# Optimization experiments

Measured on AMD Instinct MI355X. Metric: run time of the kernel, lower is better.

## Reference

```python
import jax, jax.numpy as jnp
import numpy as np

B, S, H = 1, 2048, 2048
NH, KVH = 32, 8
HD = H // NH
GROUPS = NH // KVH
ROPE_THETA = 10000.0


def _rope(x):
    # x: (b, s, heads, head_dim); HF-style rotate-half RoPE
    d = x.shape[-1]
    s = x.shape[1]
    inv_freq = 1.0 / (ROPE_THETA ** (jnp.arange(0, d, 2, dtype=jnp.float32) / d))
    t = jnp.arange(s, dtype=jnp.float32)
    freqs = jnp.einsum('s,f->sf', t, inv_freq)          # (s, d/2)
    emb = jnp.concatenate([freqs, freqs], axis=-1)       # (s, d)
    cos = jnp.cos(emb)[None, :, None, :].astype(x.dtype)
    sin = jnp.sin(emb)[None, :, None, :].astype(x.dtype)
    x1, x2 = x[..., : d // 2], x[..., d // 2:]
    rot = jnp.concatenate([-x2, x1], axis=-1)
    return x * cos + rot * sin


def setup_inputs() -> dict:
    key = jax.random.key(0)
    ks = jax.random.split(key, 6)
    scale = 0.02
    hidden_states = jax.random.normal(ks[0], (B, S, H), dtype=jnp.float32)
    Wq = jax.random.normal(ks[1], (H, NH, HD), dtype=jnp.float32) * scale
    Wk = jax.random.normal(ks[2], (H, KVH, HD), dtype=jnp.float32) * scale
    Wv = jax.random.normal(ks[3], (H, KVH, HD), dtype=jnp.float32) * scale
    Wo = jax.random.normal(ks[4], (H, H), dtype=jnp.float32) * scale
    # causal additive mask (b,1,s,s): 0 on/below diagonal, large negative above
    causal = jnp.tril(jnp.ones((S, S), dtype=bool))
    attention_mask = jnp.where(causal, 0.0, -1e9).astype(jnp.float32)[None, None]
    return {"hidden_states": hidden_states, "Wq": Wq, "Wk": Wk, "Wv": Wv,
            "Wo": Wo, "attention_mask": attention_mask}


def reference(hidden_states, Wq, Wk, Wv, Wo, attention_mask):
    b, s, _ = hidden_states.shape
    q = jnp.einsum('bsh,hnd->bsnd', hidden_states, Wq)   # (b,s,NH,HD)
    k = jnp.einsum('bsh,hnd->bsnd', hidden_states, Wk)   # (b,s,KVH,HD)
    v = jnp.einsum('bsh,hnd->bsnd', hidden_states, Wv)   # (b,s,KVH,HD)
    q = _rope(q)
    k = _rope(k)
    # GQA: tile kv heads along head axis (tf.tile semantics)
    k = jnp.tile(k, (1, 1, GROUPS, 1))                   # (b,s,NH,HD)
    v = jnp.tile(v, (1, 1, GROUPS, 1))
    # scores: 'aecd,abcd->acbe' -> (b, heads, q_len, k_len)
    scores = jnp.einsum('bend,bqnd->bnqe', k, q) / jnp.sqrt(
        jnp.asarray(HD, dtype=q.dtype))
    scores = scores + attention_mask
    scores = jnp.maximum(scores, jnp.finfo(scores.dtype).min)
    probs = jax.nn.softmax(scores, axis=-1)
    attn = jnp.einsum('bnqe,bend->bqnd', probs, v)       # (b,s,NH,HD)
    attn = attn.reshape(b, s, H)
    return jnp.einsum('bsh,hd->bsd', attn, Wo)
```

## Files before the change

kernel.cpp:

```cpp
#include <hip/hip_runtime.h>
#include <stdint.h>

typedef unsigned short u16;
typedef uint32_t u32;
typedef uint64_t u64;
typedef float f32x4 __attribute__((ext_vector_type(4)));
typedef float f32x16 __attribute__((ext_vector_type(16)));
typedef __bf16 bf16x8 __attribute__((ext_vector_type(8)));

#define S_LEN 2048
#define HID 2048
#define N_HEADS 32
#define KV_HEADS 8
#define HEAD_DIM 64
#define QKV_COLS 3072
#define QSCALE 0.18033688011112042f

__device__ __forceinline__ u16 f2b(float x) {
  union { float f; uint32_t u; } c; c.f = x;
  uint32_t u = (c.u + 0x7fffu + ((c.u >> 16) & 1u)) >> 16;
  return (u16)u;
}
__device__ __forceinline__ float b2f(u16 v) {
  union { uint32_t u; float f; } c; c.u = ((uint32_t)v) << 16;
  return c.f;
}
__device__ __forceinline__ u32 pkbf(float e, float o) {
  union { float f; u32 u; } a, b; a.f = e; b.f = o;
  return __builtin_amdgcn_perm(b.u, a.u, 0x07060302u);
}

#define GLL16(gptr, lptr)                                                      \
  __builtin_amdgcn_global_load_lds(                                            \
      (__attribute__((address_space(1))) void*)(gptr),                         \
      (__attribute__((address_space(3))) void*)(lptr), 16, 0, 0)

__global__ __launch_bounds__(256) void prep_fused(const float* __restrict__ Wq,
                                                  const float* __restrict__ Wk,
                                                  const float* __restrict__ Wv,
                                                  const float* __restrict__ Wo,
                                                  const float* __restrict__ hs,
                                                  u16* __restrict__ WqkvT,
                                                  u16* __restrict__ WoT,
                                                  u16* __restrict__ X) {
  const int b = blockIdx.x;
  const int t = threadIdx.x;
  if (b < 10240) {
    __shared__ float tile[32][33];
    const float* in;
    u16* out;
    int C, bx, by;
    if (b < 4096) { in = Wq; out = WqkvT; C = 2048; bx = b & 63; by = b >> 6; }
    else if (b < 5120) { int bb = b - 4096; in = Wk; out = WqkvT + 2048 * 2048; C = 512; bx = bb & 15; by = bb >> 4; }
    else if (b < 6144) { int bb = b - 5120; in = Wv; out = WqkvT + 2048 * 2048 + 512 * 2048; C = 512; bx = bb & 15; by = bb >> 4; }
    else { int bb = b - 6144; in = Wo; out = WoT; C = 2048; bx = bb & 63; by = bb >> 6; }
    const int tx = t & 31, ty = t >> 5;
    const int c0 = bx * 32, r0 = by * 32;
#pragma unroll
    for (int i = 0; i < 32; i += 8)
      tile[ty + i][tx] = in[(size_t)(r0 + ty + i) * C + c0 + tx];
    __syncthreads();
#pragma unroll
    for (int i = 0; i < 32; i += 8)
      out[(size_t)(c0 + ty + i) * 2048 + r0 + tx] = f2b(tile[tx][ty + i]);
  } else {
    int i = (b - 10240) * 256 + t;
    float4 v = reinterpret_cast<const float4*>(hs)[i];
    ushort4 o;
    o.x = f2b(v.x); o.y = f2b(v.y); o.z = f2b(v.z); o.w = f2b(v.w);
    reinterpret_cast<ushort4*>(X)[i] = o;
  }
}

__global__ void transpose_bf16(const u16* __restrict__ in, int istride,
                               u16* __restrict__ out, int R, int C) {
  __shared__ u16 tile[32][33];
  int c0 = blockIdx.x * 32, r0 = blockIdx.y * 32;
  int tx = threadIdx.x, ty = threadIdx.y;
#pragma unroll
  for (int i = 0; i < 32; i += 8)
    tile[ty + i][tx] = in[(size_t)(r0 + ty + i) * istride + c0 + tx];
  __syncthreads();
#pragma unroll
  for (int i = 0; i < 32; i += 8)
    out[(size_t)(c0 + ty + i) * R + r0 + tx] = tile[tx][ty + i];
}

__global__ __launch_bounds__(256) void gemm128s(const u16* __restrict__ A,
                                                const u16* __restrict__ BT,
                                                float* __restrict__ Cp,
                                                int M, int N, int K, int ksplit) {
  __shared__ __align__(16) u16 As[128 * 64];
  __shared__ __align__(16) u16 Bs[128 * 64];
  const int t = threadIdx.x;
  const int w = t >> 6, l = t & 63;
  const int lr = l & 15, lk = l >> 4;
  const int wr = w >> 1, wc = w & 1;
  const int m0 = blockIdx.x * 128, n0 = blockIdx.y * 128;
  const int z = blockIdx.z;
  const int kspan = K / ksplit;
  const int kBeg = z * kspan, kEnd = kBeg + kspan;
  Cp += (size_t)z * M * N;

  f32x4 acc[4][4];
#pragma unroll
  for (int m = 0; m < 4; ++m)
#pragma unroll
    for (int n = 0; n < 4; ++n)
      acc[m][n] = (f32x4){0.f, 0.f, 0.f, 0.f};

  const u16* aSrc = A + (size_t)(m0 + t / 8) * K + (t % 8) * 8;
  const u16* bSrc = BT + (size_t)(n0 + t / 8) * K + (t % 8) * 8;
  char* aDst = (char*)As + w * 1024;
  char* bDst = (char*)Bs + w * 1024;

  for (int k0 = kBeg; k0 < kEnd; k0 += 64) {
#pragma unroll
    for (int i = 0; i < 4; ++i)
      GLL16(aSrc + (size_t)i * 32 * K + k0, aDst + i * 4096);
#pragma unroll
    for (int i = 0; i < 4; ++i)
      GLL16(bSrc + (size_t)i * 32 * K + k0, bDst + i * 4096);
    __syncthreads();
#pragma unroll
    for (int kk = 0; kk < 2; ++kk) {
      bf16x8 af[4], bfr[4];
#pragma unroll
      for (int m = 0; m < 4; ++m)
        af[m] = *(const bf16x8*)&As[(wr * 64 + m * 16 + lr) * 64 + kk * 32 + lk * 8];
#pragma unroll
      for (int n = 0; n < 4; ++n)
        bfr[n] = *(const bf16x8*)&Bs[(wc * 64 + n * 16 + lr) * 64 + kk * 32 + lk * 8];
#pragma unroll
      for (int m = 0; m < 4; ++m)
#pragma unroll
        for (int n = 0; n < 4; ++n)
          acc[m][n] = __builtin_amdgcn_mfma_f32_16x16x32_bf16(af[m], bfr[n], acc[m][n], 0, 0, 0);
    }
    __syncthreads();
  }
#pragma unroll
  for (int m = 0; m < 4; ++m)
#pragma unroll
    for (int n = 0; n < 4; ++n) {
      int row0 = m0 + wr * 64 + m * 16 + lk * 4;
      int col = n0 + wc * 64 + n * 16 + lr;
#pragma unroll
      for (int r = 0; r < 4; ++r)
        Cp[(size_t)(row0 + r) * N + col] = acc[m][n][r];
    }
}

__global__ __launch_bounds__(256) void post_qkv(const float* __restrict__ P0,
                                                const float* __restrict__ P1,
                                                u16* __restrict__ QKV) {
  int idx = blockIdx.x * 256 + threadIdx.x;
  int s = idx / 1536, j = idx - s * 1536;
  const float* r0 = P0 + (size_t)s * QKV_COLS;
  const float* r1 = P1 + (size_t)s * QKV_COLS;
  u16* o = QKV + (size_t)s * QKV_COLS;
  if (j < 1280) {
    int hbase, i;
    float scale;
    if (j < 1024) { hbase = (j >> 5) * 64; i = j & 31; scale = QSCALE; }
    else { int jj = j - 1024; hbase = 2048 + (jj >> 5) * 64; i = jj & 31; scale = 1.0f; }
    int c1 = hbase + i, c2 = c1 + 32;
    float inv = __expf(-(float)i * (9.210340371976184f / 32.0f));
    float f = (float)s * inv;
    float sn, cs;
    sincosf(f, &sn, &cs);
    float x1 = r0[c1] + r1[c1], x2 = r0[c2] + r1[c2];
    o[c1] = f2b((x1 * cs - x2 * sn) * scale);
    o[c2] = f2b((x2 * cs + x1 * sn) * scale);
  } else {
    int c = 2560 + (j - 1280) * 2;
    *(u32*)(o + c) = pkbf(r0[c] + r1[c], r0[c + 1] + r1[c + 1]);
  }
}

__global__ __launch_bounds__(256) void post_out(const float* __restrict__ P0,
                                                const float* __restrict__ P1,
                                                float* __restrict__ out) {
  int i = blockIdx.x * 256 + threadIdx.x;
  float4 a = reinterpret_cast<const float4*>(P0)[i];
  float4 b = reinterpret_cast<const float4*>(P1)[i];
  a.x += b.x; a.y += b.y; a.z += b.z; a.w += b.w;
  reinterpret_cast<float4*>(out)[i] = a;
}

__global__ __launch_bounds__(256) void attn_kernel(const u16* __restrict__ QKV,
                                                   const u16* __restrict__ Vt,
                                                   u16* __restrict__ At) {
  __shared__ __align__(16) u16 scratch[4][32 * 64];
  const int t = threadIdx.x;
  const int w = t >> 6, l = t & 63;
  const int lq = l & 31;
  const int hi = l >> 5;
  const int b = blockIdx.x;
  const int qt = (b < 256) ? (63 - (b >> 3)) : ((b - 256) >> 3);
  const int head = (b & 7) * 4 + w;
  const int kvh = head & (KV_HEADS - 1);
  const int qbase = qt * 32;
  char* pb = (char*)scratch[w];
  const int swrow = lq * 128;
  const int swx = (lq & 7) << 4;

  bf16x8 qf[4];
  {
    const u16* qp = QKV + (size_t)(qbase + lq) * QKV_COLS + head * HEAD_DIM + hi * 8;
#pragma unroll
    for (int jj = 0; jj < 4; ++jj) qf[jj] = *(const bf16x8*)(qp + jj * 16);
  }
  const u16* Kb = QKV + HID + kvh * HEAD_DIM;
  const u16* Vb = Vt + (size_t)(kvh * HEAD_DIM) * S_LEN;

  f32x16 oacc0, oacc1;
#pragma unroll
  for (int i = 0; i < 16; ++i) { oacc0[i] = 0.f; oacc1[i] = 0.f; }
  float m_run = -1e30f;
  float l_run = 0.f;

  auto loadK = [&](int kv0, bf16x8* k0, bf16x8* k1) {
    const u16* kp = Kb + (size_t)(kv0 + lq) * QKV_COLS + hi * 8;
#pragma unroll
    for (int jj = 0; jj < 4; ++jj) {
      k0[jj] = *(const bf16x8*)(kp + jj * 16);
      k1[jj] = *(const bf16x8*)(kp + (size_t)32 * QKV_COLS + jj * 16);
    }
  };

  auto tile = [&](int kv0, const bf16x8* kf0, const bf16x8* kf1, bool mask0, bool mask1) {
    f32x16 s0, s1;
#pragma unroll
    for (int i = 0; i < 16; ++i) { s0[i] = 0.f; s1[i] = 0.f; }
#pragma unroll
    for (int jj = 0; jj < 4; ++jj)
      s0 = __builtin_amdgcn_mfma_f32_32x32x16_bf16(kf0[jj], qf[jj], s0, 0, 0, 0);
#pragma unroll
    for (int jj = 0; jj < 4; ++jj)
      s1 = __builtin_amdgcn_mfma_f32_32x32x16_bf16(kf1[jj], qf[jj], s1, 0, 0, 0);
    bf16x8 vf0[4], vf1[4];
    const u16* vp = Vb + (size_t)lq * S_LEN + kv0 + hi * 8;
#pragma unroll
    for (int ks = 0; ks < 4; ++ks) {
      vf0[ks] = *(const bf16x8*)(vp + ks * 16);
      vf1[ks] = *(const bf16x8*)(vp + (size_t)32 * S_LEN + ks * 16);
    }
    if (mask0) {
      const int c = kv0 - qbase;
#pragma unroll
      for (int r = 0; r < 16; ++r) {
        int kvr = (r & 3) + 8 * (r >> 2) + 4 * hi + c;
        s0[r] = (kvr > lq) ? -1e30f : s0[r];
      }
    }
    if (mask1) {
      const int c = kv0 + 32 - qbase;
#pragma unroll
      for (int r = 0; r < 16; ++r) {
        int kvr = (r & 3) + 8 * (r >> 2) + 4 * hi + c;
        s1[r] = (kvr > lq) ? -1e30f : s1[r];
      }
    }
    float mx[16];
#pragma unroll
    for (int r = 0; r < 16; ++r) mx[r] = fmaxf(s0[r], s1[r]);
#pragma unroll
    for (int st = 8; st >= 1; st >>= 1)
#pragma unroll
      for (int r = 0; r < st; ++r) mx[r] = fmaxf(mx[r], mx[r + st]);
    float pm = mx[0];
    pm = fmaxf(pm, __shfl_xor(pm, 32));
    if (!__all(pm <= m_run + 8.f)) {
      float mnew = fmaxf(m_run, pm);
      float esc = exp2f(m_run - mnew);
      m_run = mnew;
      l_run *= esc;
#pragma unroll
      for (int i = 0; i < 16; ++i) { oacc0[i] *= esc; oacc1[i] *= esc; }
    }
#pragma unroll
    for (int r = 0; r < 16; ++r) {
      s0[r] = exp2f(s0[r] - m_run);
      s1[r] = exp2f(s1[r] - m_run);
    }
    float ls[16];
#pragma unroll
    for (int r = 0; r < 16; ++r) ls[r] = s0[r] + s1[r];
#pragma unroll
    for (int st = 8; st >= 1; st >>= 1)
#pragma unroll
      for (int r = 0; r < st; ++r) ls[r] += ls[r + st];
    l_run += ls[0];
#pragma unroll
    for (int sb = 0; sb < 2; ++sb)
#pragma unroll
      for (int g = 0; g < 4; ++g) {
        u32 w0 = sb ? pkbf(s1[4 * g + 0], s1[4 * g + 1]) : pkbf(s0[4 * g + 0], s0[4 * g + 1]);
        u32 w1 = sb ? pkbf(s1[4 * g + 2], s1[4 * g + 3]) : pkbf(s0[4 * g + 2], s0[4 * g + 3]);
        int kvb2 = (32 * sb + 8 * g + 4 * hi) * 2;
        *(u64*)(pb + swrow + (kvb2 ^ swx)) = (u64)w0 | ((u64)w1 << 32);
      }
    asm volatile("s_waitcnt lgkmcnt(0)" ::: "memory");
    __builtin_amdgcn_sched_barrier(0);
    bf16x8 pa[4];
#pragma unroll
    for (int ks = 0; ks < 4; ++ks)
      pa[ks] = *(const bf16x8*)(pb + swrow + ((32 * ks + 16 * hi) ^ swx));
    asm volatile("" ::: "memory");
#pragma unroll
    for (int ks = 0; ks < 4; ++ks) {
      oacc0 = __builtin_amdgcn_mfma_f32_32x32x16_bf16(vf0[ks], pa[ks], oacc0, 0, 0, 0);
      oacc1 = __builtin_amdgcn_mfma_f32_32x32x16_bf16(vf1[ks], pa[ks], oacc1, 0, 0, 0);
    }
  };

  const int NTF = qt >> 1;
  bf16x8 ka0[4], ka1[4], kb0[4], kb1[4];
  loadK(0, ka0, ka1);
  int tl = 0;
  for (; tl + 2 <= NTF; tl += 2) {
    loadK((tl + 1) * 64, kb0, kb1);
    tile(tl * 64, ka0, ka1, false, false);
    loadK((tl + 2) * 64, ka0, ka1);
    tile((tl + 1) * 64, kb0, kb1, false, false);
  }
  if (tl < NTF) {
    loadK((tl + 1) * 64, kb0, kb1);
    tile(tl * 64, ka0, ka1, false, false);
    tile(NTF * 64, kb0, kb1, (qt & 1) == 0, true);
  } else {
    tile(NTF * 64, ka0, ka1, (qt & 1) == 0, true);
  }

  float l_tot = l_run + __shfl_xor(l_run, 32);
  float inv = 1.0f / l_tot;
  asm volatile("" ::: "memory");
#pragma unroll
  for (int dt = 0; dt < 2; ++dt) {
#pragma unroll
    for (int j = 0; j < 8; ++j) {
      int d = dt * 32 + 2 * (j & 1) + 8 * (j >> 1) + 4 * hi;
      float e = (dt ? oacc1[2 * j] : oacc0[2 * j]) * inv;
      float o = (dt ? oacc1[2 * j + 1] : oacc0[2 * j + 1]) * inv;
      *(u32*)(pb + swrow + ((d * 2) ^ swx)) = pkbf(e, o);
    }
  }
  asm volatile("s_waitcnt lgkmcnt(0)" ::: "memory");
  __builtin_amdgcn_sched_barrier(0);
#pragma unroll
  for (int pass = 0; pass < 4; ++pass) {
    int qq = pass * 8 + (l >> 3);
    int coff = (l & 7) * 16;
    f32x4 v = *(const f32x4*)(pb + qq * 128 + (coff ^ ((qq & 7) << 4)));
    *(f32x4*)&At[(size_t)(qbase + qq) * HID + head * HEAD_DIM + (l & 7) * 8] = v;
  }
}

extern "C" void kernel_launch(void* const* d_in, const int* in_sizes, int n_in,
                              void* d_out, int out_size, void* d_ws, size_t ws_size,
                              hipStream_t stream) {
  const float* hs = (const float*)d_in[0];
  const float* Wq = (const float*)d_in[1];
  const float* Wk = (const float*)d_in[2];
  const float* Wv = (const float*)d_in[3];
  const float* Wo = (const float*)d_in[4];

  char* ws = (char*)d_ws;
  const size_t MB = 1024 * 1024;
  u16* X      = (u16*)(ws + 0 * MB);
  u16* WqkvT  = (u16*)(ws + 8 * MB);
  u16* WoT    = (u16*)(ws + 20 * MB);
  u16* QKV    = (u16*)(ws + 28 * MB);
  u16* Vt     = (u16*)(ws + 40 * MB);
  u16* At     = (u16*)(ws + 42 * MB);
  float* QKVp = (float*)(ws + 50 * MB);
  float* Op   = (float*)(ws + 50 * MB);

  prep_fused<<<14336, 256, 0, stream>>>(Wq, Wk, Wv, Wo, hs, WqkvT, WoT, X);
  gemm128s<<<dim3(16, 24, 2), 256, 0, stream>>>(X, WqkvT, QKVp, 2048, QKV_COLS, 2048, 2);
  post_qkv<<<12288, 256, 0, stream>>>(QKVp, QKVp + (size_t)2048 * QKV_COLS, QKV);
  transpose_bf16<<<dim3(16, 64), dim3(32, 8), 0, stream>>>(QKV + HID + 512, QKV_COLS, Vt, 2048, 512);
  attn_kernel<<<dim3(512), 256, 0, stream>>>(QKV, Vt, At);
  gemm128s<<<dim3(16, 16, 2), 256, 0, stream>>>(At, WoT, Op, 2048, 2048, 2048, 2);
  post_out<<<4096, 256, 0, stream>>>(Op, Op + (size_t)2048 * 2048, (float*)d_out);
}
```

Before: 293.0 us.

## Split KV loop across four waves per head with LDS softmax merge

Before, each block ran four heads, one per wave, and each wave walked the full causal KV range for its 32-query tile. Now each block handles one (query tile, head) pair, and its four waves take interleaved 64-key tiles. Partial max, sum and output accumulators are merged through LDS by wave 0 (a split-K flash-decoding style reduction). The grid grows from 512 to 2048 blocks, which shortens the critical path of long causal rows and balances load better. The cost is extra LDS traffic, a block barrier, a serial merge on one wave, and loss of the explicit K register double-buffering.

```diff
diff --git a/kernel.cpp b/kernel.cpp
--- a/kernel.cpp
+++ b/kernel.cpp
@@ -191,17 +191,18 @@
 __global__ __launch_bounds__(256) void attn_kernel(const u16* __restrict__ QKV,
                                                    const u16* __restrict__ Vt,
                                                    u16* __restrict__ At) {
-  __shared__ __align__(16) u16 scratch[4][32 * 64];
+  __shared__ __align__(16) char slot[4][8192];
+  __shared__ float ml[4][2][64];
   const int t = threadIdx.x;
   const int w = t >> 6, l = t & 63;
   const int lq = l & 31;
   const int hi = l >> 5;
   const int b = blockIdx.x;
-  const int qt = (b < 256) ? (63 - (b >> 3)) : ((b - 256) >> 3);
-  const int head = (b & 7) * 4 + w;
+  const int qt = 63 - (b >> 5);
+  const int head = b & 31;
   const int kvh = head & (KV_HEADS - 1);
   const int qbase = qt * 32;
-  char* pb = (char*)scratch[w];
+  char* pb = (char*)slot[w];
   const int swrow = lq * 128;
   const int swx = (lq & 7) << 4;
 
@@ -220,16 +221,19 @@
   float m_run = -1e30f;
   float l_run = 0.f;
 
-  auto loadK = [&](int kv0, bf16x8* k0, bf16x8* k1) {
+  const int NT = (qt >> 1) + 1;
+  for (int j = w; j < NT; j += 4) {
+    const int kv0 = j * 64;
+    const bool tail = (j == NT - 1);
+    const bool mask0 = tail && ((qt & 1) == 0);
+    const bool mask1 = tail;
     const u16* kp = Kb + (size_t)(kv0 + lq) * QKV_COLS + hi * 8;
+    bf16x8 kf0[4], kf1[4];
 #pragma unroll
     for (int jj = 0; jj < 4; ++jj) {
-      k0[jj] = *(const bf16x8*)(kp + jj * 16);
-      k1[jj] = *(const bf16x8*)(kp + (size_t)32 * QKV_COLS + jj * 16);
-    }
-  };
-
-  auto tile = [&](int kv0, const bf16x8* kf0, const bf16x8* kf1, bool mask0, bool mask1) {
+      kf0[jj] = *(const bf16x8*)(kp + jj * 16);
+      kf1[jj] = *(const bf16x8*)(kp + (size_t)32 * QKV_COLS + jj * 16);
+    }
     f32x16 s0, s1;
 #pragma unroll
     for (int i = 0; i < 16; ++i) { s0[i] = 0.f; s1[i] = 0.f; }
@@ -313,36 +317,54 @@
       oacc0 = __builtin_amdgcn_mfma_f32_32x32x16_bf16(vf0[ks], pa[ks], oacc0, 0, 0, 0);
       oacc1 = __builtin_amdgcn_mfma_f32_32x32x16_bf16(vf1[ks], pa[ks], oacc1, 0, 0, 0);
     }
-  };
-
-  const int NTF = qt >> 1;
-  bf16x8 ka0[4], ka1[4], kb0[4], kb1[4];
-  loadK(0, ka0, ka1);
-  int tl = 0;
-  for (; tl + 2 <= NTF; tl += 2) {
-    loadK((tl + 1) * 64, kb0, kb1);
-    tile(tl * 64, ka0, ka1, false, false);
-    loadK((tl + 2) * 64, ka0, ka1);
-    tile((tl + 1) * 64, kb0, kb1, false, false);
-  }
-  if (tl < NTF) {
-    loadK((tl + 1) * 64, kb0, kb1);
-    tile(tl * 64, ka0, ka1, false, false);
-    tile(NTF * 64, kb0, kb1, (qt & 1) == 0, true);
-  } else {
-    tile(NTF * 64, ka0, ka1, (qt & 1) == 0, true);
-  }
-
-  float l_tot = l_run + __shfl_xor(l_run, 32);
-  float inv = 1.0f / l_tot;
-  asm volatile("" ::: "memory");
+  }
+
+  ml[w][0][l] = m_run;
+  ml[w][1][l] = l_run;
+  {
+    f32x4* os = (f32x4*)slot[w];
+#pragma unroll
+    for (int i = 0; i < 4; ++i) {
+      os[i * 64 + l] = (f32x4){oacc0[4 * i], oacc0[4 * i + 1], oacc0[4 * i + 2], oacc0[4 * i + 3]};
+      os[(4 + i) * 64 + l] = (f32x4){oacc1[4 * i], oacc1[4 * i + 1], oacc1[4 * i + 2], oacc1[4 * i + 3]};
+    }
+  }
+  __syncthreads();
+  if (w != 0) return;
+
+  float mw[4], sc[4];
+#pragma unroll
+  for (int w2 = 0; w2 < 4; ++w2) mw[w2] = ml[w2][0][l];
+  float m = fmaxf(fmaxf(mw[0], mw[1]), fmaxf(mw[2], mw[3]));
+  float ltot = 0.f;
+#pragma unroll
+  for (int w2 = 0; w2 < 4; ++w2) {
+    sc[w2] = exp2f(mw[w2] - m);
+    float lw = ml[w2][1][l];
+    float lx = ml[w2][1][l ^ 32];
+    ltot += (lw + lx) * sc[w2];
+  }
+  float inv = 1.0f / ltot;
+  f32x4 O[8];
+#pragma unroll
+  for (int i = 0; i < 8; ++i) O[i] = (f32x4){0.f, 0.f, 0.f, 0.f};
+#pragma unroll
+  for (int w2 = 0; w2 < 4; ++w2) {
+    const f32x4* os = (const f32x4*)slot[w2];
+#pragma unroll
+    for (int i = 0; i < 8; ++i) {
+      f32x4 v = os[i * 64 + l];
+      O[i][0] += v[0] * sc[w2]; O[i][1] += v[1] * sc[w2];
+      O[i][2] += v[2] * sc[w2]; O[i][3] += v[3] * sc[w2];
+    }
+  }
 #pragma unroll
   for (int dt = 0; dt < 2; ++dt) {
 #pragma unroll
     for (int j = 0; j < 8; ++j) {
       int d = dt * 32 + 2 * (j & 1) + 8 * (j >> 1) + 4 * hi;
-      float e = (dt ? oacc1[2 * j] : oacc0[2 * j]) * inv;
-      float o = (dt ? oacc1[2 * j + 1] : oacc0[2 * j + 1]) * inv;
+      float e = O[dt * 4 + (j >> 1)][2 * (j & 1)] * inv;
+      float o = O[dt * 4 + (j >> 1)][2 * (j & 1) + 1] * inv;
       *(u32*)(pb + swrow + ((d * 2) ^ swx)) = pkbf(e, o);
     }
   }
@@ -381,7 +403,7 @@
   gemm128s<<<dim3(16, 24, 2), 256, 0, stream>>>(X, WqkvT, QKVp, 2048, QKV_COLS, 2048, 2);
   post_qkv<<<12288, 256, 0, stream>>>(QKVp, QKVp + (size_t)2048 * QKV_COLS, QKV);
   transpose_bf16<<<dim3(16, 64), dim3(32, 8), 0, stream>>>(QKV + HID + 512, QKV_COLS, Vt, 2048, 512);
-  attn_kernel<<<dim3(512), 256, 0, stream>>>(QKV, Vt, At);
+  attn_kernel<<<dim3(2048), 256, 0, stream>>>(QKV, Vt, At);
   gemm128s<<<dim3(16, 16, 2), 256, 0, stream>>>(At, WoT, Op, 2048, 2048, 2048, 2);
   post_out<<<4096, 256, 0, stream>>>(Op, Op + (size_t)2048 * 2048, (float*)d_out);
 }
```

Result: faster. 285.6 us (-2.6%).
